# Optimization experiments

Measured on AMD Instinct MI355X. Metric: run time of the kernel, lower is better.

## Reference

```python
import jax, jax.numpy as jnp
import numpy as np

B, T, D, DE, S, P = 16384, 2, 1024, 512, 4, 4  # batch, tasks, inp_dim, expt_dim, share, specific


def setup_inputs() -> dict:
    key = jax.random.key(0)
    ks = jax.random.split(key, 8)
    sc = 0.02
    return {
        "x0": jax.random.normal(ks[0], (B, D), jnp.float32),
        "x1": jax.random.normal(ks[1], (B, D), jnp.float32),
        "W_share": jax.random.normal(ks[2], (S, D, DE), jnp.float32) * sc,
        "b_share": jnp.zeros((S, DE), jnp.float32),
        "W_spcf": jax.random.normal(ks[3], (T, P, D, DE), jnp.float32) * sc,
        "b_spcf": jnp.zeros((T, P, DE), jnp.float32),
        "W_gate": jax.random.normal(ks[4], (T, D, S + P), jnp.float32) * sc,
        "b_gate": jnp.zeros((T, S + P), jnp.float32),
    }


def reference(x0, x1, W_share, b_share, W_spcf, b_spcf, W_gate, b_gate):
    # cat_x: [B, T, D]
    x = jnp.stack([x0, x1], axis=1)
    # per-task gate over all S+P experts: [B, T, S+P]
    gates = jax.nn.softmax(jnp.einsum("btd,tde->bte", x, W_gate) + b_gate, axis=-1)
    # shared experts applied to every task's input: [B, T, S, DE]
    share = jax.nn.relu(jnp.einsum("btd,sdf->btsf", x, W_share) + b_share[None, None])
    # task-specific experts applied to their own task input: [B, T, P, DE]
    spcf = jax.nn.relu(jnp.einsum("btd,tpdf->btpf", x, W_spcf) + b_spcf[None])
    experts = jnp.concatenate([share, spcf], axis=2)  # [B, T, S+P, DE]
    # softmax-gated mixture: [B, T, DE] (== list of per-task [B, DE] in the original)
    return jnp.einsum("bte,btef->btf", gates, experts)
```

## Files before the change

kernel.cpp:

```cpp
#include <hip/hip_runtime.h>
#include <stdint.h>

#define kB  16384
#define kD  1024
#define kDE 512

typedef __bf16 bf16x8 __attribute__((ext_vector_type(8)));
typedef float  f32x4  __attribute__((ext_vector_type(4)));

__device__ __forceinline__ unsigned short f2bf(float f) {
    union { float f; unsigned u; } v; v.f = f;
    unsigned r = v.u + 0x7FFFu + ((v.u >> 16) & 1u);
    return (unsigned short)(r >> 16);
}

__device__ __forceinline__ void async16(unsigned short* lds, const unsigned short* g) {
    __builtin_amdgcn_global_load_lds(
        (const __attribute__((address_space(1))) unsigned int*)g,
        (__attribute__((address_space(3))) unsigned int*)lds, 16, 0, 0);
}

__global__ __launch_bounds__(256) void prep_w(const float* __restrict__ Wsh,
                                              const float* __restrict__ Wsp,
                                              unsigned short* __restrict__ Wt) {
    __shared__ float tile[64][65];
    const int slot = blockIdx.z;
    const int k0 = blockIdx.x * 64;
    const int n0 = blockIdx.y * 64;
    const float* src = (slot < 4) ? (Wsh + (size_t)slot * kD * kDE)
                                  : (Wsp + (size_t)(slot - 4) * kD * kDE);
    const int tid = threadIdx.x;
    const int lr = tid >> 4, lc = (tid & 15) * 4;
#pragma unroll
    for (int i = 0; i < 4; i++) {
        const float4 v = *(const float4*)&src[(size_t)(k0 + lr + i * 16) * kDE + n0 + lc];
        tile[lr + i * 16][lc + 0] = v.x;
        tile[lr + i * 16][lc + 1] = v.y;
        tile[lr + i * 16][lc + 2] = v.z;
        tile[lr + i * 16][lc + 3] = v.w;
    }
    __syncthreads();
    const int wn = tid >> 2, wk = (tid & 3) * 16;
    unsigned short* dst = Wt + (size_t)slot * kDE * kD + (size_t)(n0 + wn) * kD + k0 + wk;
#pragma unroll
    for (int j = 0; j < 4; j++) {
        ushort4 h;
        h.x = f2bf(tile[wk + j * 4 + 0][wn]);
        h.y = f2bf(tile[wk + j * 4 + 1][wn]);
        h.z = f2bf(tile[wk + j * 4 + 2][wn]);
        h.w = f2bf(tile[wk + j * 4 + 3][wn]);
        *(ushort4*)(dst + j * 4) = h;
    }
}

__global__ __launch_bounds__(256) void conv_gate(
    const float* __restrict__ x0, const float* __restrict__ x1,
    const float* __restrict__ Wg, const float* __restrict__ bg,
    unsigned short* __restrict__ xb, float* __restrict__ g) {
    const int wid = threadIdx.x >> 6, lane = threadIdx.x & 63;
    const int r = blockIdx.x * 4 + wid;
    const int t = r >> 14, b = r & 16383;
    const float* xrow = (t ? x1 : x0) + (size_t)b * kD;
    unsigned short* xbrow = xb + (size_t)(t * kB + b) * kD;
    const float* Wgt = Wg + t * kD * 8;
    float p[8] = {0.f,0.f,0.f,0.f,0.f,0.f,0.f,0.f};
#pragma unroll
    for (int it = 0; it < 4; it++) {
        const int d0 = it * 256 + lane * 4;
        const float4 v = *(const float4*)(xrow + d0);
        ushort4 h;
        h.x = f2bf(v.x); h.y = f2bf(v.y); h.z = f2bf(v.z); h.w = f2bf(v.w);
        *(ushort4*)(xbrow + d0) = h;
        const float xv[4] = {v.x, v.y, v.z, v.w};
#pragma unroll
        for (int j = 0; j < 4; j++) {
            const float* wrow = Wgt + (size_t)(d0 + j) * 8;
            const float4 wa = *(const float4*)wrow;
            const float4 wb = *(const float4*)(wrow + 4);
            p[0] += xv[j] * wa.x; p[1] += xv[j] * wa.y;
            p[2] += xv[j] * wa.z; p[3] += xv[j] * wa.w;
            p[4] += xv[j] * wb.x; p[5] += xv[j] * wb.y;
            p[6] += xv[j] * wb.z; p[7] += xv[j] * wb.w;
        }
    }
#pragma unroll
    for (int e = 0; e < 8; e++) {
        float v = p[e];
#pragma unroll
        for (int s = 1; s < 64; s <<= 1) v += __shfl_xor(v, s, 64);
        p[e] = v;
    }
    float lg[8];
#pragma unroll
    for (int e = 0; e < 8; e++) lg[e] = p[e] + bg[t * 8 + e];
    float mx = lg[0];
#pragma unroll
    for (int e = 1; e < 8; e++) mx = fmaxf(mx, lg[e]);
    float s = 0.f;
#pragma unroll
    for (int e = 0; e < 8; e++) { lg[e] = __expf(lg[e] - mx); s += lg[e]; }
    const float inv = 1.f / s;
    if (lane == 0) {
        float* gp = g + (size_t)(t * kB + b) * 8;
        float4 g0 = {lg[0]*inv, lg[1]*inv, lg[2]*inv, lg[3]*inv};
        float4 g1 = {lg[4]*inv, lg[5]*inv, lg[6]*inv, lg[7]*inv};
        *(float4*)gp = g0;
        *(float4*)(gp + 4) = g1;
    }
}

__global__ __launch_bounds__(512, 2) void moe_gemm(
    const unsigned short* __restrict__ xb, const unsigned short* __restrict__ Wt,
    const float* __restrict__ g, const float* __restrict__ bsh,
    const float* __restrict__ bsp, float* __restrict__ out) {
    __shared__ __align__(16) unsigned short As[2][128 * 64];
    __shared__ __align__(16) unsigned short Bs[2][8 * 64 * 64];

    const int bid = blockIdx.x;
    const int swz = (bid & 7) * 256 + (bid >> 3);
    const int ct = swz & 7;
    const int rt = (swz >> 3) & 127;
    const int t  = swz >> 10;
    const int n0 = ct * 64;

    const int tid = threadIdx.x, wid = tid >> 6, lane = tid & 63;
    const int wr = wid >> 2, wc = wid & 3;

    const int swzChunk = ((lane & 7) ^ ((lane >> 3) & 7)) * 8;
    const unsigned short* aSrc = xb + (size_t)t * kB * kD +
        (size_t)(rt * 128 + wid * 16 + (lane >> 3)) * kD + swzChunk;
    const int slot = (wid < 4) ? wid : (4 + t * 4 + (wid - 4));
    const unsigned short* bSrc = Wt + (size_t)slot * kDE * kD +
        (size_t)(n0 + (lane >> 3)) * kD + swzChunk;

    const int rAbase = (wr * 64 + (lane & 15)) * 64;
    const int bOff   = (wc * 16 + (lane & 15)) * 64;
    const int lx     = lane & 7;
    const int kg     = lane >> 4;

    f32x4 acc[8][4];
#pragma unroll
    for (int e = 0; e < 8; e++)
#pragma unroll
        for (int m = 0; m < 4; m++) acc[e][m] = (f32x4){0.f, 0.f, 0.f, 0.f};

#define STAGE(buf, kt)                                                        \
    {                                                                         \
        const int k0_ = (kt) * 64;                                            \
        _Pragma("unroll")                                                     \
        for (int i = 0; i < 2; i++)                                           \
            async16(&As[buf][wid * 1024 + i * 512], aSrc + k0_ + i * 8 * kD); \
        _Pragma("unroll")                                                     \
        for (int j = 0; j < 8; j++)                                           \
            async16(&Bs[buf][wid * 4096 + j * 512], bSrc + k0_ + j * 8 * kD); \
    }

#define COMPUTE(buf)                                                          \
    {                                                                         \
        _Pragma("unroll")                                                     \
        for (int ks = 0; ks < 2; ks++) {                                      \
            const int p8 = ((ks * 4 + kg) ^ lx) * 8;                          \
            bf16x8 af[4];                                                     \
            _Pragma("unroll")                                                 \
            for (int m = 0; m < 4; m++)                                       \
                af[m] = *(const bf16x8*)&As[buf][rAbase + m * 1024 + p8];     \
            _Pragma("unroll")                                                 \
            for (int e = 0; e < 8; e++) {                                     \
                bf16x8 bf = *(const bf16x8*)&Bs[buf][e * 4096 + bOff + p8];   \
                _Pragma("unroll")                                             \
                for (int m = 0; m < 4; m++)                                   \
                    acc[e][m] = __builtin_amdgcn_mfma_f32_16x16x32_bf16(      \
                        af[m], bf, acc[e][m], 0, 0, 0);                       \
            }                                                                 \
        }                                                                     \
    }

    STAGE(0, 0);
    for (int kt2 = 0; kt2 < 8; ++kt2) {
        STAGE(1, kt2 * 2 + 1);
        asm volatile("s_waitcnt vmcnt(10)" ::: "memory");
        __builtin_amdgcn_s_barrier();
        COMPUTE(0);
        __builtin_amdgcn_s_barrier();
        STAGE(0, (kt2 * 2 + 2) & 15);
        asm volatile("s_waitcnt vmcnt(10)" ::: "memory");
        __builtin_amdgcn_s_barrier();
        COMPUTE(1);
        __builtin_amdgcn_s_barrier();
    }
    asm volatile("s_waitcnt vmcnt(0)" ::: "memory");

#undef STAGE
#undef COMPUTE

    const int col = n0 + wc * 16 + (lane & 15);
    float bv[8];
#pragma unroll
    for (int e = 0; e < 8; e++)
        bv[e] = (e < 4) ? bsh[e * kDE + col] : bsp[(t * 4 + (e - 4)) * kDE + col];

#pragma unroll
    for (int m = 0; m < 4; m++) {
        const int r0 = rt * 128 + wr * 64 + m * 16 + kg * 4;
#pragma unroll
        for (int q = 0; q < 4; q++) {
            const float* gp = g + ((size_t)t * kB + r0 + q) * 8;
            const float4 ga = *(const float4*)gp;
            const float4 gb = *(const float4*)(gp + 4);
            float s = ga.x * fmaxf(acc[0][m][q] + bv[0], 0.f)
                    + ga.y * fmaxf(acc[1][m][q] + bv[1], 0.f)
                    + ga.z * fmaxf(acc[2][m][q] + bv[2], 0.f)
                    + ga.w * fmaxf(acc[3][m][q] + bv[3], 0.f)
                    + gb.x * fmaxf(acc[4][m][q] + bv[4], 0.f)
                    + gb.y * fmaxf(acc[5][m][q] + bv[5], 0.f)
                    + gb.z * fmaxf(acc[6][m][q] + bv[6], 0.f)
                    + gb.w * fmaxf(acc[7][m][q] + bv[7], 0.f);
            out[((size_t)(r0 + q) * 2 + t) * kDE + col] = s;
        }
    }
}

extern "C" void kernel_launch(void* const* d_in, const int* in_sizes, int n_in,
                              void* d_out, int out_size, void* d_ws, size_t ws_size,
                              hipStream_t stream) {
    const float* x0  = (const float*)d_in[0];
    const float* x1  = (const float*)d_in[1];
    const float* Wsh = (const float*)d_in[2];
    const float* bsh = (const float*)d_in[3];
    const float* Wsp = (const float*)d_in[4];
    const float* bsp = (const float*)d_in[5];
    const float* Wg  = (const float*)d_in[6];
    const float* bg  = (const float*)d_in[7];
    float* out = (float*)d_out;

    char* ws = (char*)d_ws;
    unsigned short* xb = (unsigned short*)ws;
    unsigned short* Wt = (unsigned short*)(ws + 67108864);
    float* g  = (float*)(ws + 67108864 + 12582912);

    prep_w<<<dim3(16, 8, 12), dim3(256), 0, stream>>>(Wsh, Wsp, Wt);
    conv_gate<<<dim3(8192), dim3(256), 0, stream>>>(x0, x1, Wg, bg, xb, g);
    moe_gemm<<<dim3(2048), dim3(512), 0, stream>>>(xb, Wt, g, bsh, bsp, out);
}
```

Before: 410.7 us.

## Fuse prep kernels and interleave staged loads with MFMA sub-blocks in GEMM

The two preprocessing kernels (weight transpose/convert and input convert plus gate softmax) are merged into one launch, with blocks split by index, to save a launch and the gap between them. The GEMM main loop is rebuilt as a finer software pipeline. Each k-step is split into four MFMA groups, and the next tile's global-to-LDS loads are spread across those groups. Loads are divided unevenly between two warp halves, with per-half vmcnt waits, and s_setprio raises priority around the MFMA bursts. This aims to overlap memory traffic with matrix math better, but it adds more barriers and relies on exact hand-counted waitcnt values for correctness.

```diff
diff --git a/kernel.cpp b/kernel.cpp
--- a/kernel.cpp
+++ b/kernel.cpp
@@ -20,45 +20,47 @@
         (__attribute__((address_space(3))) unsigned int*)lds, 16, 0, 0);
 }
 
-__global__ __launch_bounds__(256) void prep_w(const float* __restrict__ Wsh,
-                                              const float* __restrict__ Wsp,
-                                              unsigned short* __restrict__ Wt) {
-    __shared__ float tile[64][65];
-    const int slot = blockIdx.z;
-    const int k0 = blockIdx.x * 64;
-    const int n0 = blockIdx.y * 64;
-    const float* src = (slot < 4) ? (Wsh + (size_t)slot * kD * kDE)
-                                  : (Wsp + (size_t)(slot - 4) * kD * kDE);
-    const int tid = threadIdx.x;
-    const int lr = tid >> 4, lc = (tid & 15) * 4;
-#pragma unroll
-    for (int i = 0; i < 4; i++) {
-        const float4 v = *(const float4*)&src[(size_t)(k0 + lr + i * 16) * kDE + n0 + lc];
-        tile[lr + i * 16][lc + 0] = v.x;
-        tile[lr + i * 16][lc + 1] = v.y;
-        tile[lr + i * 16][lc + 2] = v.z;
-        tile[lr + i * 16][lc + 3] = v.w;
-    }
-    __syncthreads();
-    const int wn = tid >> 2, wk = (tid & 3) * 16;
-    unsigned short* dst = Wt + (size_t)slot * kDE * kD + (size_t)(n0 + wn) * kD + k0 + wk;
-#pragma unroll
-    for (int j = 0; j < 4; j++) {
-        ushort4 h;
-        h.x = f2bf(tile[wk + j * 4 + 0][wn]);
-        h.y = f2bf(tile[wk + j * 4 + 1][wn]);
-        h.z = f2bf(tile[wk + j * 4 + 2][wn]);
-        h.w = f2bf(tile[wk + j * 4 + 3][wn]);
-        *(ushort4*)(dst + j * 4) = h;
-    }
-}
-
-__global__ __launch_bounds__(256) void conv_gate(
+__global__ __launch_bounds__(256) void prep_all(
+    const float* __restrict__ Wsh, const float* __restrict__ Wsp,
+    unsigned short* __restrict__ Wt,
     const float* __restrict__ x0, const float* __restrict__ x1,
     const float* __restrict__ Wg, const float* __restrict__ bg,
     unsigned short* __restrict__ xb, float* __restrict__ g) {
+    if (blockIdx.x < 1536) {
+        __shared__ float tile[64][65];
+        const int idx = blockIdx.x;
+        const int slot = idx >> 7;
+        const int rem = idx & 127;
+        const int k0 = (rem & 15) * 64;
+        const int n0 = (rem >> 4) * 64;
+        const float* src = (slot < 4) ? (Wsh + (size_t)slot * kD * kDE)
+                                      : (Wsp + (size_t)(slot - 4) * kD * kDE);
+        const int tid = threadIdx.x;
+        const int lr = tid >> 4, lc = (tid & 15) * 4;
+#pragma unroll
+        for (int i = 0; i < 4; i++) {
+            const float4 v = *(const float4*)&src[(size_t)(k0 + lr + i * 16) * kDE + n0 + lc];
+            tile[lr + i * 16][lc + 0] = v.x;
+            tile[lr + i * 16][lc + 1] = v.y;
+            tile[lr + i * 16][lc + 2] = v.z;
+            tile[lr + i * 16][lc + 3] = v.w;
+        }
+        __syncthreads();
+        const int wn = tid >> 2, wk = (tid & 3) * 16;
+        unsigned short* dst = Wt + (size_t)slot * kDE * kD + (size_t)(n0 + wn) * kD + k0 + wk;
+#pragma unroll
+        for (int j = 0; j < 4; j++) {
+            ushort4 h;
+            h.x = f2bf(tile[wk + j * 4 + 0][wn]);
+            h.y = f2bf(tile[wk + j * 4 + 1][wn]);
+            h.z = f2bf(tile[wk + j * 4 + 2][wn]);
+            h.w = f2bf(tile[wk + j * 4 + 3][wn]);
+            *(ushort4*)(dst + j * 4) = h;
+        }
+        return;
+    }
     const int wid = threadIdx.x >> 6, lane = threadIdx.x & 63;
-    const int r = blockIdx.x * 4 + wid;
+    const int r = (blockIdx.x - 1536) * 4 + wid;
     const int t = r >> 14, b = r & 16383;
     const float* xrow = (t ? x1 : x0) + (size_t)b * kD;
     unsigned short* xbrow = xb + (size_t)(t * kB + b) * kD;
@@ -125,6 +127,7 @@
 
     const int tid = threadIdx.x, wid = tid >> 6, lane = tid & 63;
     const int wr = wid >> 2, wc = wid & 3;
+    const bool early = (wid < 4);
 
     const int swzChunk = ((lane & 7) ^ ((lane >> 3) & 7)) * 8;
     const unsigned short* aSrc = xb + (size_t)t * kB * kD +
@@ -144,54 +147,101 @@
 #pragma unroll
         for (int m = 0; m < 4; m++) acc[e][m] = (f32x4){0.f, 0.f, 0.f, 0.f};
 
-#define STAGE(buf, kt)                                                        \
-    {                                                                         \
-        const int k0_ = (kt) * 64;                                            \
-        _Pragma("unroll")                                                     \
-        for (int i = 0; i < 2; i++)                                           \
-            async16(&As[buf][wid * 1024 + i * 512], aSrc + k0_ + i * 8 * kD); \
-        _Pragma("unroll")                                                     \
-        for (int j = 0; j < 8; j++)                                           \
-            async16(&Bs[buf][wid * 4096 + j * 512], bSrc + k0_ + j * 8 * kD); \
-    }
-
-#define COMPUTE(buf)                                                          \
-    {                                                                         \
-        _Pragma("unroll")                                                     \
-        for (int ks = 0; ks < 2; ks++) {                                      \
-            const int p8 = ((ks * 4 + kg) ^ lx) * 8;                          \
-            bf16x8 af[4];                                                     \
-            _Pragma("unroll")                                                 \
-            for (int m = 0; m < 4; m++)                                       \
-                af[m] = *(const bf16x8*)&As[buf][rAbase + m * 1024 + p8];     \
-            _Pragma("unroll")                                                 \
-            for (int e = 0; e < 8; e++) {                                     \
-                bf16x8 bf = *(const bf16x8*)&Bs[buf][e * 4096 + bOff + p8];   \
-                _Pragma("unroll")                                             \
-                for (int m = 0; m < 4; m++)                                   \
-                    acc[e][m] = __builtin_amdgcn_mfma_f32_16x16x32_bf16(      \
-                        af[m], bf, acc[e][m], 0, 0, 0);                       \
-            }                                                                 \
-        }                                                                     \
-    }
-
-    STAGE(0, 0);
+    bf16x8 af[4], bfr[4];
+
+#define S_A(buf, ktn)                                                          \
+    async16(&As[buf][wid * 1024 + 0 * 512], aSrc + (ktn) * 64 + 0 * 8 * kD);   \
+    async16(&As[buf][wid * 1024 + 1 * 512], aSrc + (ktn) * 64 + 1 * 8 * kD);
+
+#define S_B(buf, ktn, j)                                                       \
+    async16(&Bs[buf][wid * 4096 + (j) * 512], bSrc + (ktn) * 64 + (j) * 8 * kD);
+
+#define R_A(buf, ks)                                                           \
+    _Pragma("unroll")                                                          \
+    for (int m = 0; m < 4; m++)                                                \
+        af[m] = *(const bf16x8*)&As[buf][rAbase + m * 1024 +                   \
+                                         ((((ks) * 4 + kg) ^ lx) << 3)];
+
+#define R_B4(buf, ks, e0)                                                      \
+    _Pragma("unroll")                                                          \
+    for (int i = 0; i < 4; i++)                                                \
+        bfr[i] = *(const bf16x8*)&Bs[buf][((e0) + i) * 4096 + bOff +           \
+                                          ((((ks) * 4 + kg) ^ lx) << 3)];
+
+#define MM4(e0)                                                                \
+    asm volatile("s_waitcnt lgkmcnt(0)" ::: "memory");                         \
+    __builtin_amdgcn_sched_barrier(0);                                         \
+    __builtin_amdgcn_s_setprio(1);                                             \
+    _Pragma("unroll")                                                          \
+    for (int i = 0; i < 4; i++)                                                \
+        _Pragma("unroll")                                                      \
+        for (int m = 0; m < 4; m++)                                            \
+            acc[(e0) + i][m] = __builtin_amdgcn_mfma_f32_16x16x32_bf16(        \
+                af[m], bfr[i], acc[(e0) + i][m], 0, 0, 0);                     \
+    __builtin_amdgcn_s_setprio(0);
+
+#define STEP(cur, nxt, ktn)                                                    \
+    {                                                                          \
+                                                            \
+        R_A(cur, 0); R_B4(cur, 0, 0);                                          \
+        if (early) {                                                           \
+            S_A(nxt, ktn); S_B(nxt, ktn, 0); S_B(nxt, ktn, 1);                 \
+        } else {                                                               \
+            S_A(nxt, ktn);                                                     \
+            asm volatile("s_waitcnt vmcnt(2)" ::: "memory");                   \
+        }                                                                      \
+        __builtin_amdgcn_s_barrier();                                          \
+        MM4(0);                                                                \
+                                                \
+        R_B4(cur, 0, 4);                                                       \
+        if (early) {                                                           \
+            S_B(nxt, ktn, 2); S_B(nxt, ktn, 3);                                \
+            S_B(nxt, ktn, 4); S_B(nxt, ktn, 5);                                \
+        }                                                                      \
+        __builtin_amdgcn_s_barrier();                                          \
+        MM4(4);                                                                \
+                                                            \
+        R_A(cur, 1); R_B4(cur, 1, 0);                                          \
+        if (early) {                                                           \
+            S_B(nxt, ktn, 6); S_B(nxt, ktn, 7);                                \
+        } else {                                                               \
+            S_B(nxt, ktn, 0); S_B(nxt, ktn, 1);                                \
+            S_B(nxt, ktn, 2); S_B(nxt, ktn, 3);                                \
+        }                                                                      \
+        __builtin_amdgcn_s_barrier();                                          \
+        MM4(0);                                                                \
+                      \
+        R_B4(cur, 1, 4);                                                       \
+        if (!early) {                                                          \
+            S_B(nxt, ktn, 4); S_B(nxt, ktn, 5);                                \
+            S_B(nxt, ktn, 6); S_B(nxt, ktn, 7);                                \
+        }                                                                      \
+        __builtin_amdgcn_s_barrier();                                          \
+        MM4(4);                                                                \
+        if (early) { asm volatile("s_waitcnt vmcnt(0)" ::: "memory"); }        \
+        else       { asm volatile("s_waitcnt vmcnt(8)" ::: "memory"); }        \
+        __builtin_amdgcn_s_barrier();                                          \
+    }
+
+    S_A(0, 0);
+    S_B(0, 0, 0); S_B(0, 0, 1); S_B(0, 0, 2); S_B(0, 0, 3);
+    S_B(0, 0, 4); S_B(0, 0, 5); S_B(0, 0, 6); S_B(0, 0, 7);
+    if (early) { asm volatile("s_waitcnt vmcnt(0)" ::: "memory"); }
+    else       { asm volatile("s_waitcnt vmcnt(8)" ::: "memory"); }
+    __builtin_amdgcn_s_barrier();
+
     for (int kt2 = 0; kt2 < 8; ++kt2) {
-        STAGE(1, kt2 * 2 + 1);
-        asm volatile("s_waitcnt vmcnt(10)" ::: "memory");
-        __builtin_amdgcn_s_barrier();
-        COMPUTE(0);
-        __builtin_amdgcn_s_barrier();
-        STAGE(0, (kt2 * 2 + 2) & 15);
-        asm volatile("s_waitcnt vmcnt(10)" ::: "memory");
-        __builtin_amdgcn_s_barrier();
-        COMPUTE(1);
-        __builtin_amdgcn_s_barrier();
+        STEP(0, 1, kt2 * 2 + 1)
+        STEP(1, 0, (kt2 * 2 + 2) & 15)
     }
     asm volatile("s_waitcnt vmcnt(0)" ::: "memory");
 
-#undef STAGE
-#undef COMPUTE
+#undef S_A
+#undef S_B
+#undef R_A
+#undef R_B4
+#undef MM4
+#undef STEP
 
     const int col = n0 + wc * 16 + (lane & 15);
     float bv[8];
@@ -238,7 +288,6 @@
     unsigned short* Wt = (unsigned short*)(ws + 67108864);
     float* g  = (float*)(ws + 67108864 + 12582912);
 
-    prep_w<<<dim3(16, 8, 12), dim3(256), 0, stream>>>(Wsh, Wsp, Wt);
-    conv_gate<<<dim3(8192), dim3(256), 0, stream>>>(x0, x1, Wg, bg, xb, g);
+    prep_all<<<dim3(9728), dim3(256), 0, stream>>>(Wsh, Wsp, Wt, x0, x1, Wg, bg, xb, g);
     moe_gemm<<<dim3(2048), dim3(512), 0, stream>>>(xb, Wt, g, bsh, bsp, out);
 }
```

Measured after the change: 415.4 us. Within noise of the previous version (+1.1%).

## Halve GEMM row tile and K step to raise occupancy in MoE kernel

Applied to the files above, without the earlier changes.

The fused MoE GEMM now uses 64-row by 64-column tiles (over 8 experts) with a K step of 32 in place of 128 rows and K step 64. This halves the accumulators per thread and shrinks LDS, so launch bounds allow 4 blocks per CU and the grid doubles to 4096 blocks. The LDS swizzle is redone for 32-wide K rows, and sched_barrier pins the compute phase between block barriers. The cost is less reuse of B tiles per block, so more global and LDS traffic for weights, plus twice as many barrier round-trips per K.

```diff
diff --git a/kernel.cpp b/kernel.cpp
--- a/kernel.cpp
+++ b/kernel.cpp
@@ -109,89 +109,98 @@
     }
 }
 
-__global__ __launch_bounds__(512, 2) void moe_gemm(
+__global__ __launch_bounds__(512, 4) void moe_gemm(
     const unsigned short* __restrict__ xb, const unsigned short* __restrict__ Wt,
     const float* __restrict__ g, const float* __restrict__ bsh,
     const float* __restrict__ bsp, float* __restrict__ out) {
-    __shared__ __align__(16) unsigned short As[2][128 * 64];
-    __shared__ __align__(16) unsigned short Bs[2][8 * 64 * 64];
+    __shared__ __align__(16) unsigned short As[2][64 * 32];
+    __shared__ __align__(16) unsigned short Bs[2][8 * 64 * 32];
 
     const int bid = blockIdx.x;
-    const int swz = (bid & 7) * 256 + (bid >> 3);
-    const int ct = swz & 7;
-    const int rt = (swz >> 3) & 127;
-    const int t  = swz >> 10;
-    const int n0 = ct * 64;
+    const int w = (bid & 7) * 512 + (bid >> 3);
+    const int ct = w & 7;
+    const int rw = (w >> 3) & 255;
+    const int t  = w >> 11;
+    const int rowBase = rw * 64, n0 = ct * 64;
 
     const int tid = threadIdx.x, wid = tid >> 6, lane = tid & 63;
     const int wr = wid >> 2, wc = wid & 3;
-
-    const int swzChunk = ((lane & 7) ^ ((lane >> 3) & 7)) * 8;
-    const unsigned short* aSrc = xb + (size_t)t * kB * kD +
-        (size_t)(rt * 128 + wid * 16 + (lane >> 3)) * kD + swzChunk;
+    const bool hasA = (wid < 4);
+
+    const int dSt = (lane & 7) ^ (lane >> 3);
+    const unsigned short* aS = xb + (size_t)t * kB * kD +
+        (size_t)(rowBase + wid * 16 + (lane >> 3) * 2 + (dSt >> 2)) * kD + (dSt & 3) * 8;
     const int slot = (wid < 4) ? wid : (4 + t * 4 + (wid - 4));
-    const unsigned short* bSrc = Wt + (size_t)slot * kDE * kD +
-        (size_t)(n0 + (lane >> 3)) * kD + swzChunk;
-
-    const int rAbase = (wr * 64 + (lane & 15)) * 64;
-    const int bOff   = (wc * 16 + (lane & 15)) * 64;
-    const int lx     = lane & 7;
-    const int kg     = lane >> 4;
-
-    f32x4 acc[8][4];
+    const unsigned short* bS = Wt + (size_t)slot * kDE * kD +
+        (size_t)(n0 + (lane >> 3) * 2 + (dSt >> 2)) * kD + (dSt & 3) * 8;
+
+    const int l15h = (lane & 15) >> 1;
+    const int swR = (((lane & 1) * 4 + (lane >> 4)) ^ l15h);
+    const int aRd = wr * 1024 + l15h * 64 + swR * 8;
+    const int bRd = wc * 512  + l15h * 64 + swR * 8;
+    const int kg  = lane >> 4;
+
+    f32x4 acc[8][2];
 #pragma unroll
     for (int e = 0; e < 8; e++)
 #pragma unroll
-        for (int m = 0; m < 4; m++) acc[e][m] = (f32x4){0.f, 0.f, 0.f, 0.f};
-
-#define STAGE(buf, kt)                                                        \
-    {                                                                         \
-        const int k0_ = (kt) * 64;                                            \
-        _Pragma("unroll")                                                     \
-        for (int i = 0; i < 2; i++)                                           \
-            async16(&As[buf][wid * 1024 + i * 512], aSrc + k0_ + i * 8 * kD); \
-        _Pragma("unroll")                                                     \
-        for (int j = 0; j < 8; j++)                                           \
-            async16(&Bs[buf][wid * 4096 + j * 512], bSrc + k0_ + j * 8 * kD); \
-    }
-
-#define COMPUTE(buf)                                                          \
-    {                                                                         \
-        _Pragma("unroll")                                                     \
-        for (int ks = 0; ks < 2; ks++) {                                      \
-            const int p8 = ((ks * 4 + kg) ^ lx) * 8;                          \
-            bf16x8 af[4];                                                     \
-            _Pragma("unroll")                                                 \
-            for (int m = 0; m < 4; m++)                                       \
-                af[m] = *(const bf16x8*)&As[buf][rAbase + m * 1024 + p8];     \
-            _Pragma("unroll")                                                 \
-            for (int e = 0; e < 8; e++) {                                     \
-                bf16x8 bf = *(const bf16x8*)&Bs[buf][e * 4096 + bOff + p8];   \
-                _Pragma("unroll")                                             \
-                for (int m = 0; m < 4; m++)                                   \
-                    acc[e][m] = __builtin_amdgcn_mfma_f32_16x16x32_bf16(      \
-                        af[m], bf, acc[e][m], 0, 0, 0);                       \
-            }                                                                 \
-        }                                                                     \
-    }
+        for (int m = 0; m < 2; m++) acc[e][m] = (f32x4){0.f, 0.f, 0.f, 0.f};
+
+#define STAGE(buf, ktn)                                                        \
+    {                                                                          \
+        if (hasA) async16(&As[buf][wid * 512], aS + (ktn) * 32);               \
+        _Pragma("unroll")                                                      \
+        for (int j = 0; j < 4; j++)                                            \
+            async16(&Bs[buf][wid * 2048 + j * 512],                            \
+                    bS + (size_t)j * 16 * kD + (ktn) * 32);                    \
+    }
+
+#define WAITP                                                                  \
+    if (hasA) { asm volatile("s_waitcnt vmcnt(5)" ::: "memory"); }             \
+    else      { asm volatile("s_waitcnt vmcnt(4)" ::: "memory"); }
+
+#define COMPUTE(buf)                                                           \
+    {                                                                          \
+        bf16x8 af[2], bfr[4];                                                  \
+        _Pragma("unroll")                                                      \
+        for (int m = 0; m < 2; m++)                                            \
+            af[m] = *(const bf16x8*)&As[buf][aRd + m * 512];                   \
+        _Pragma("unroll")                                                      \
+        for (int c = 0; c < 2; c++) {                                          \
+            _Pragma("unroll")                                                  \
+            for (int i = 0; i < 4; i++)                                        \
+                bfr[i] = *(const bf16x8*)&Bs[buf][bRd + (c * 4 + i) * 2048];   \
+            _Pragma("unroll")                                                  \
+            for (int i = 0; i < 4; i++)                                        \
+                _Pragma("unroll")                                              \
+                for (int m = 0; m < 2; m++)                                    \
+                    acc[c * 4 + i][m] = __builtin_amdgcn_mfma_f32_16x16x32_bf16( \
+                        af[m], bfr[i], acc[c * 4 + i][m], 0, 0, 0);            \
+        }                                                                      \
+    }
+
+#define COMPUTE_PINNED(buf)                                                    \
+    __builtin_amdgcn_s_barrier();                                              \
+    __builtin_amdgcn_sched_barrier(0);                                         \
+    COMPUTE(buf);                                                              \
+    __builtin_amdgcn_sched_barrier(0);                                         \
+    __builtin_amdgcn_s_barrier();
 
     STAGE(0, 0);
-    for (int kt2 = 0; kt2 < 8; ++kt2) {
+    for (int kt2 = 0; kt2 < 16; ++kt2) {
         STAGE(1, kt2 * 2 + 1);
-        asm volatile("s_waitcnt vmcnt(10)" ::: "memory");
-        __builtin_amdgcn_s_barrier();
-        COMPUTE(0);
-        __builtin_amdgcn_s_barrier();
-        STAGE(0, (kt2 * 2 + 2) & 15);
-        asm volatile("s_waitcnt vmcnt(10)" ::: "memory");
-        __builtin_amdgcn_s_barrier();
-        COMPUTE(1);
-        __builtin_amdgcn_s_barrier();
+        WAITP;
+        COMPUTE_PINNED(0);
+        STAGE(0, (kt2 * 2 + 2) & 31);
+        WAITP;
+        COMPUTE_PINNED(1);
     }
     asm volatile("s_waitcnt vmcnt(0)" ::: "memory");
 
 #undef STAGE
+#undef WAITP
 #undef COMPUTE
+#undef COMPUTE_PINNED
 
     const int col = n0 + wc * 16 + (lane & 15);
     float bv[8];
@@ -200,8 +209,8 @@
         bv[e] = (e < 4) ? bsh[e * kDE + col] : bsp[(t * 4 + (e - 4)) * kDE + col];
 
 #pragma unroll
-    for (int m = 0; m < 4; m++) {
-        const int r0 = rt * 128 + wr * 64 + m * 16 + kg * 4;
+    for (int m = 0; m < 2; m++) {
+        const int r0 = rowBase + wr * 32 + m * 16 + kg * 4;
 #pragma unroll
         for (int q = 0; q < 4; q++) {
             const float* gp = g + ((size_t)t * kB + r0 + q) * 8;
@@ -240,5 +249,5 @@
 
     prep_w<<<dim3(16, 8, 12), dim3(256), 0, stream>>>(Wsh, Wsp, Wt);
     conv_gate<<<dim3(8192), dim3(256), 0, stream>>>(x0, x1, Wg, bg, xb, g);
-    moe_gemm<<<dim3(2048), dim3(512), 0, stream>>>(xb, Wt, g, bsh, bsp, out);
-}
+    moe_gemm<<<dim3(4096), dim3(512), 0, stream>>>(xb, Wt, g, bsh, bsp, out);
+}
```

Result: slower. 495.4 us (+20.6%).

## Pre-swizzle weights into MFMA fragment layout and load B directly into registers

Applied to the files above, without the earlier changes.

The weight prep kernel now writes bf16 weights in a per-lane MFMA fragment order, so each wave can load its B operands straight from global memory into registers with one 16-byte load per expert per k-step. This removes the B tile from LDS, cutting LDS traffic and footprint, and leaves only A staged through LDS. The B loads are software-pipelined in two register sets that are refilled after use. Each wave now fetches its own B fragments from global or L2 with no sharing through LDS, and register pressure goes up.

```diff
diff --git a/kernel.cpp b/kernel.cpp
--- a/kernel.cpp
+++ b/kernel.cpp
@@ -20,36 +20,41 @@
         (__attribute__((address_space(3))) unsigned int*)lds, 16, 0, 0);
 }
 
-__global__ __launch_bounds__(256) void prep_w(const float* __restrict__ Wsh,
-                                              const float* __restrict__ Wsp,
-                                              unsigned short* __restrict__ Wt) {
-    __shared__ float tile[64][65];
-    const int slot = blockIdx.z;
-    const int k0 = blockIdx.x * 64;
-    const int n0 = blockIdx.y * 64;
-    const float* src = (slot < 4) ? (Wsh + (size_t)slot * kD * kDE)
-                                  : (Wsp + (size_t)(slot - 4) * kD * kDE);
+__global__ __launch_bounds__(256) void prep_wf(const float* __restrict__ Wsh,
+                                               const float* __restrict__ Wsp,
+                                               unsigned short* __restrict__ Wf) {
+    __shared__ float tile[32][512];
+    const int kc = blockIdx.x;
+    const int slot = blockIdx.y;
+    const float* src = ((slot < 4) ? (Wsh + (size_t)slot * kD * kDE)
+                                   : (Wsp + (size_t)(slot - 4) * kD * kDE))
+                       + (size_t)kc * 32 * kDE;
     const int tid = threadIdx.x;
-    const int lr = tid >> 4, lc = (tid & 15) * 4;
-#pragma unroll
-    for (int i = 0; i < 4; i++) {
-        const float4 v = *(const float4*)&src[(size_t)(k0 + lr + i * 16) * kDE + n0 + lc];
-        tile[lr + i * 16][lc + 0] = v.x;
-        tile[lr + i * 16][lc + 1] = v.y;
-        tile[lr + i * 16][lc + 2] = v.z;
-        tile[lr + i * 16][lc + 3] = v.w;
+#pragma unroll
+    for (int i = 0; i < 16; i++) {
+        const int idx = i * 256 + tid;
+        const int row = idx >> 7;
+        const int c4 = (idx & 127) << 2;
+        const float4 v = *(const float4*)&src[(size_t)row * kDE + c4];
+        tile[row][c4 + 0] = v.x; tile[row][c4 + 1] = v.y;
+        tile[row][c4 + 2] = v.z; tile[row][c4 + 3] = v.w;
     }
     __syncthreads();
-    const int wn = tid >> 2, wk = (tid & 3) * 16;
-    unsigned short* dst = Wt + (size_t)slot * kDE * kD + (size_t)(n0 + wn) * kD + k0 + wk;
-#pragma unroll
-    for (int j = 0; j < 4; j++) {
-        ushort4 h;
-        h.x = f2bf(tile[wk + j * 4 + 0][wn]);
-        h.y = f2bf(tile[wk + j * 4 + 1][wn]);
-        h.z = f2bf(tile[wk + j * 4 + 2][wn]);
-        h.w = f2bf(tile[wk + j * 4 + 3][wn]);
-        *(ushort4*)(dst + j * 4) = h;
+    const int nt = tid >> 3;
+    const int l0 = (tid & 7) * 8;
+    unsigned short* dst = Wf + ((size_t)(slot * 32 + kc) * 32 + nt) * 512;
+#pragma unroll
+    for (int li = 0; li < 8; li++) {
+        const int l = l0 + li;
+        const int col = nt * 16 + (l & 15);
+        const int kb = (l >> 4) * 8;
+        ushort4 ha, hb;
+        ha.x = f2bf(tile[kb + 0][col]); ha.y = f2bf(tile[kb + 1][col]);
+        ha.z = f2bf(tile[kb + 2][col]); ha.w = f2bf(tile[kb + 3][col]);
+        hb.x = f2bf(tile[kb + 4][col]); hb.y = f2bf(tile[kb + 5][col]);
+        hb.z = f2bf(tile[kb + 6][col]); hb.w = f2bf(tile[kb + 7][col]);
+        *(ushort4*)(dst + l * 8) = ha;
+        *(ushort4*)(dst + l * 8 + 4) = hb;
     }
 }
 
@@ -110,11 +115,10 @@
 }
 
 __global__ __launch_bounds__(512, 2) void moe_gemm(
-    const unsigned short* __restrict__ xb, const unsigned short* __restrict__ Wt,
+    const unsigned short* __restrict__ xb, const unsigned short* __restrict__ Wf,
     const float* __restrict__ g, const float* __restrict__ bsh,
     const float* __restrict__ bsp, float* __restrict__ out) {
     __shared__ __align__(16) unsigned short As[2][128 * 64];
-    __shared__ __align__(16) unsigned short Bs[2][8 * 64 * 64];
 
     const int bid = blockIdx.x;
     const int swz = (bid & 7) * 256 + (bid >> 3);
@@ -129,14 +133,18 @@
     const int swzChunk = ((lane & 7) ^ ((lane >> 3) & 7)) * 8;
     const unsigned short* aSrc = xb + (size_t)t * kB * kD +
         (size_t)(rt * 128 + wid * 16 + (lane >> 3)) * kD + swzChunk;
-    const int slot = (wid < 4) ? wid : (4 + t * 4 + (wid - 4));
-    const unsigned short* bSrc = Wt + (size_t)slot * kDE * kD +
-        (size_t)(n0 + (lane >> 3)) * kD + swzChunk;
-
     const int rAbase = (wr * 64 + (lane & 15)) * 64;
-    const int bOff   = (wc * 16 + (lane & 15)) * 64;
-    const int lx     = lane & 7;
-    const int kg     = lane >> 4;
+    const int lx = lane & 7;
+    const int kg = lane >> 4;
+
+    const int nt = ct * 4 + wc;
+    const bf16x8* wfL = (const bf16x8*)Wf + lane;
+    int soff[8];
+#pragma unroll
+    for (int e = 0; e < 8; e++) {
+        const int slotE = (e < 4) ? e : (4 + t * 4 + (e - 4));
+        soff[e] = slotE * 65536 + nt * 64;
+    }
 
     f32x4 acc[8][4];
 #pragma unroll
@@ -144,54 +152,61 @@
 #pragma unroll
         for (int m = 0; m < 4; m++) acc[e][m] = (f32x4){0.f, 0.f, 0.f, 0.f};
 
-#define STAGE(buf, kt)                                                        \
-    {                                                                         \
-        const int k0_ = (kt) * 64;                                            \
-        _Pragma("unroll")                                                     \
-        for (int i = 0; i < 2; i++)                                           \
-            async16(&As[buf][wid * 1024 + i * 512], aSrc + k0_ + i * 8 * kD); \
-        _Pragma("unroll")                                                     \
-        for (int j = 0; j < 8; j++)                                           \
-            async16(&Bs[buf][wid * 4096 + j * 512], bSrc + k0_ + j * 8 * kD); \
-    }
-
-#define COMPUTE(buf)                                                          \
-    {                                                                         \
-        _Pragma("unroll")                                                     \
-        for (int ks = 0; ks < 2; ks++) {                                      \
-            const int p8 = ((ks * 4 + kg) ^ lx) * 8;                          \
-            bf16x8 af[4];                                                     \
-            _Pragma("unroll")                                                 \
-            for (int m = 0; m < 4; m++)                                       \
-                af[m] = *(const bf16x8*)&As[buf][rAbase + m * 1024 + p8];     \
-            _Pragma("unroll")                                                 \
-            for (int e = 0; e < 8; e++) {                                     \
-                bf16x8 bf = *(const bf16x8*)&Bs[buf][e * 4096 + bOff + p8];   \
-                _Pragma("unroll")                                             \
-                for (int m = 0; m < 4; m++)                                   \
-                    acc[e][m] = __builtin_amdgcn_mfma_f32_16x16x32_bf16(      \
-                        af[m], bf, acc[e][m], 0, 0, 0);                       \
-            }                                                                 \
-        }                                                                     \
-    }
-
-    STAGE(0, 0);
+    bf16x8 b0[8], b1[8], af[4];
+
+#define STAGE_A(buf, ktn)                                                      \
+    async16(&As[buf][wid * 1024], aSrc + (ktn) * 64);                          \
+    async16(&As[buf][wid * 1024 + 512], aSrc + (ktn) * 64 + 8 * kD);
+
+#define LOADB(dst, kc)                                                         \
+    _Pragma("unroll")                                                          \
+    for (int e = 0; e < 8; e++) dst[e] = wfL[soff[e] + (kc) * 2048];
+
+#define R_A(buf, ks)                                                           \
+    _Pragma("unroll")                                                          \
+    for (int m = 0; m < 4; m++)                                                \
+        af[m] = *(const bf16x8*)&As[buf][rAbase + m * 1024 +                   \
+                                         ((((ks) * 4 + kg) ^ lx) << 3)];
+
+#define MFMA8(bset)                                                            \
+    _Pragma("unroll")                                                          \
+    for (int e = 0; e < 8; e++)                                                \
+        _Pragma("unroll")                                                      \
+        for (int m = 0; m < 4; m++)                                            \
+            acc[e][m] = __builtin_amdgcn_mfma_f32_16x16x32_bf16(               \
+                af[m], bset[e], acc[e][m], 0, 0, 0);
+
+#define STEP(cur, nxt, ktn)                                                    \
+    {                                                                          \
+        STAGE_A(nxt, ktn);                                                     \
+        asm volatile("s_waitcnt vmcnt(18)" ::: "memory");                      \
+        __builtin_amdgcn_s_barrier();                                          \
+        __builtin_amdgcn_sched_barrier(0);                                     \
+        R_A(cur, 0);                                                           \
+        MFMA8(b0);                                                             \
+        LOADB(b0, (ktn) * 2);                                                  \
+        R_A(cur, 1);                                                           \
+        MFMA8(b1);                                                             \
+        LOADB(b1, (ktn) * 2 + 1);                                              \
+        __builtin_amdgcn_sched_barrier(0);                                     \
+        __builtin_amdgcn_s_barrier();                                          \
+    }
+
+    STAGE_A(0, 0);
+    LOADB(b0, 0);
+    LOADB(b1, 1);
+
     for (int kt2 = 0; kt2 < 8; ++kt2) {
-        STAGE(1, kt2 * 2 + 1);
-        asm volatile("s_waitcnt vmcnt(10)" ::: "memory");
-        __builtin_amdgcn_s_barrier();
-        COMPUTE(0);
-        __builtin_amdgcn_s_barrier();
-        STAGE(0, (kt2 * 2 + 2) & 15);
-        asm volatile("s_waitcnt vmcnt(10)" ::: "memory");
-        __builtin_amdgcn_s_barrier();
-        COMPUTE(1);
-        __builtin_amdgcn_s_barrier();
+        STEP(0, 1, kt2 * 2 + 1)
+        STEP(1, 0, (kt2 * 2 + 2) & 15)
     }
     asm volatile("s_waitcnt vmcnt(0)" ::: "memory");
 
-#undef STAGE
-#undef COMPUTE
+#undef STAGE_A
+#undef LOADB
+#undef R_A
+#undef MFMA8
+#undef STEP
 
     const int col = n0 + wc * 16 + (lane & 15);
     float bv[8];
@@ -235,10 +250,10 @@
 
     char* ws = (char*)d_ws;
     unsigned short* xb = (unsigned short*)ws;
-    unsigned short* Wt = (unsigned short*)(ws + 67108864);
+    unsigned short* Wf = (unsigned short*)(ws + 67108864);
     float* g  = (float*)(ws + 67108864 + 12582912);
 
-    prep_w<<<dim3(16, 8, 12), dim3(256), 0, stream>>>(Wsh, Wsp, Wt);
+    prep_wf<<<dim3(32, 12), dim3(256), 0, stream>>>(Wsh, Wsp, Wf);
     conv_gate<<<dim3(8192), dim3(256), 0, stream>>>(x0, x1, Wg, bg, xb, g);
-    moe_gemm<<<dim3(2048), dim3(512), 0, stream>>>(xb, Wt, g, bsh, bsp, out);
-}
+    moe_gemm<<<dim3(2048), dim3(512), 0, stream>>>(xb, Wf, g, bsh, bsp, out);
+}
```

Result: slower. 429.3 us (+4.5%).
